# Performance work log

Hardware: AMD Instinct MI355X
Metric: run time of the kernel (lower is better)

The kernel has to match this reference:

```python
import jax, jax.numpy as jnp
import numpy as np

V = 128      # vocab size (pad=0, sos=1, eos=2)
E = 128      # embed_dim == LSTM hidden
L = 2        # rnn_layers
B = 8192     # batch (num_samples)
T = 128      # token sequence length incl. sos/eos
PAD, SOS, EOS = 0, 1, 2


def setup_inputs() -> dict:
    key = jax.random.key(0)
    ks = jax.random.split(key, 9)
    s = 1.0 / np.sqrt(E)
    state = jax.random.normal(ks[0], (B, E), dtype=jnp.float32)
    tokens = jax.random.randint(ks[1], (B, T), 3, V)
    tokens = tokens.at[:, 0].set(SOS).at[:, -1].set(EOS)
    tok_embed = jax.random.normal(ks[2], (V, E), dtype=jnp.float32)
    W_ih = jax.random.uniform(ks[3], (L, 4 * E, E), minval=-s, maxval=s, dtype=jnp.float32)
    W_hh = jax.random.uniform(ks[4], (L, 4 * E, E), minval=-s, maxval=s, dtype=jnp.float32)
    b_ih = jax.random.uniform(ks[5], (L, 4 * E), minval=-s, maxval=s, dtype=jnp.float32)
    b_hh = jax.random.uniform(ks[6], (L, 4 * E), minval=-s, maxval=s, dtype=jnp.float32)
    W_out = jax.random.uniform(ks[7], (V, E), minval=-s, maxval=s, dtype=jnp.float32)
    b_out = jax.random.uniform(ks[8], (V,), minval=-s, maxval=s, dtype=jnp.float32)
    return {"state": state, "tokens": tokens, "tok_embed": tok_embed,
            "W_ih": W_ih, "W_hh": W_hh, "b_ih": b_ih, "b_hh": b_hh,
            "W_out": W_out, "b_out": b_out}


def _lstm(x, h0, c0, W_ih, W_hh, b_ih, b_hh):
    # x: [T, B, E] time-major; h0/c0: [L, B, E]. Gate order i,f,g,o (torch).
    n_layers = W_ih.shape[0]
    hs, cs = [], []
    for l in range(n_layers):
        Wih, Whh = W_ih[l], W_hh[l]
        b = b_ih[l] + b_hh[l]
        def step(carry, xt, Wih=Wih, Whh=Whh, b=b):
            h, c = carry
            g = xt @ Wih.T + h @ Whh.T + b            # [B, 4E]
            i, f, gg, o = jnp.split(g, 4, axis=-1)
            c = jax.nn.sigmoid(f) * c + jax.nn.sigmoid(i) * jnp.tanh(gg)
            h = jax.nn.sigmoid(o) * jnp.tanh(c)
            return (h, c), h
        (h, c), x = jax.lax.scan(step, (h0[l], c0[l]), x)
        hs.append(h)
        cs.append(c)
    return x, jnp.stack(hs), jnp.stack(cs)


def reference(state, tokens, tok_embed, W_ih, W_hh, b_ih, b_hh, W_out, b_out):
    b, e = state.shape
    n_layers = W_ih.shape[0]
    zeros = jnp.zeros((n_layers, b, e), dtype=state.dtype)
    # get_init_state: one-step LSTM over state.unsqueeze(0)
    _, h0, c0 = _lstm(state[None], zeros, zeros, W_ih, W_hh, b_ih, b_hh)
    # get_likelihood (all sequences same length -> dense, no pad tokens)
    x = tok_embed[tokens.T]                               # [T, B, E]
    out, _, _ = _lstm(x, h0, c0, W_ih, W_hh, b_ih, b_hh)  # [T, B, E]
    logits = out[:-1] @ W_out.T + b_out                   # [T-1, B, V]
    targets = tokens.T[1:]                                # [T-1, B]
    lp = jax.nn.log_softmax(logits, axis=-1)
    nll = -jnp.take_along_axis(lp, targets[..., None], axis=-1)[..., 0]
    mask = (targets != PAD).astype(nll.dtype)             # ignore_index=pad
    ll = -jnp.sum(nll * mask, axis=0)[:, None]            # [B, 1]
    return ll
```

## Files before the change

### kernel.cpp

```cpp
#include <hip/hip_runtime.h>
#include <hip/hip_bf16.h>


typedef __bf16 bf16x8 __attribute__((ext_vector_type(8)));
typedef float  f32x4  __attribute__((ext_vector_type(4)));

static __device__ __bf16 g_emb1[128 * 512];

__device__ __forceinline__ float frcp(float x) {
#if __has_builtin(__builtin_amdgcn_rcpf)
  return __builtin_amdgcn_rcpf(x);
#else
  return 1.0f / x;
#endif
}
__device__ __forceinline__ float fsig(float x) { return frcp(1.0f + __expf(-x)); }
__device__ __forceinline__ float ftanh(float x) {
  float e = __expf(2.0f * x);
  return 1.0f - 2.0f * frcp(e + 1.0f);
}

__global__ void prep_emb1(const float* __restrict__ emb, const float* __restrict__ Wih,
                          const float* __restrict__ bih, const float* __restrict__ bhh) {
  __shared__ float embS[128 * 128];
  __shared__ float wS[32 * 128];
  const int tid = threadIdx.x, bc = blockIdx.x;
  for (int i = tid; i < 128 * 32; i += 512) ((f32x4*)embS)[i] = ((const f32x4*)emb)[i];
  for (int i = tid; i < 32 * 32; i += 512)
    ((f32x4*)wS)[i] = ((const f32x4*)(Wih + bc * 32 * 128))[i];
  __syncthreads();
  const int v = tid & 127, c0 = (tid >> 7) * 8;
  const int rot = v & 31;
#pragma unroll
  for (int j = 0; j < 8; ++j) {
    int c = c0 + j;
    float s = 0.f;
    for (int k = 0; k < 128; ++k) {
      int kk = (k + rot) & 127;
      s += embS[v * 128 + kk] * wS[c * 128 + kk];
    }
    int col = bc * 32 + c;
    g_emb1[v * 512 + col] = (__bf16)(s + bih[col] + bhh[col]);
  }
}

__global__ __launch_bounds__(512, 2) void lstm_ll(
    const float* __restrict__ state, const int* __restrict__ tokens,
    const float* __restrict__ W_ih, const float* __restrict__ W_hh,
    const float* __restrict__ b_ih, const float* __restrict__ b_hh,
    const float* __restrict__ W_out, const float* __restrict__ b_out,
    float* __restrict__ out) {
  __shared__ __align__(16) __bf16 wih2L[512 * 128];
  __shared__ __align__(16) __bf16 h1L[2][32 * 128];
  __shared__ __align__(16) __bf16 h2L[32 * 128];
  __shared__ unsigned char tokL[128][32];
  __shared__ float wsum[8][32];
  __shared__ float llL[32];

  const int tid  = threadIdx.x;
  const int w    = tid >> 6;
  const int lane = tid & 63;
  const int lr   = lane & 15;
  const int lh   = lane >> 4;
  const int b0   = blockIdx.x * 32;
  const int col  = w * 16 + lr;

  for (int i = tid; i < 512 * 16; i += 512) {
    int row = i >> 4, e = (i & 15) * 8;
    const float* p = W_ih + 512 * 128 + row * 128 + e;
    f32x4 x0 = *(const f32x4*)p, x1 = *(const f32x4*)(p + 4);
    bf16x8 v;
#pragma unroll
    for (int j = 0; j < 4; ++j) { v[j] = (__bf16)x0[j]; v[4 + j] = (__bf16)x1[j]; }
    *(bf16x8*)(wih2L + row * 128 + (e ^ ((row & 7) << 3))) = v;
  }
  for (int i = tid; i < 32 * 128; i += 512) {
    int r = i & 31, t = i >> 5;
    tokL[t][r] = (unsigned char)tokens[(b0 + r) * 128 + t];
    h2L[i] = (__bf16)0.0f;
  }
  if (tid < 32) llL[tid] = 0.0f;

  auto ldw8 = [&](const float* p) -> bf16x8 {
    f32x4 x0 = *(const f32x4*)p, x1 = *(const f32x4*)(p + 4);
    bf16x8 v;
#pragma unroll
    for (int j = 0; j < 4; ++j) { v[j] = (__bf16)x0[j]; v[4 + j] = (__bf16)x1[j]; }
    return v;
  };
  bf16x8 whh1[4][4], whh2[4][4], woutF[4];
#pragma unroll
  for (int kc = 0; kc < 4; ++kc) {
#pragma unroll
    for (int gg = 0; gg < 4; ++gg) {
      whh1[kc][gg] = ldw8(W_hh + (gg * 128 + col) * 128 + kc * 32 + lh * 8);
      whh2[kc][gg] = ldw8(W_hh + 512 * 128 + (gg * 128 + col) * 128 + kc * 32 + lh * 8);
    }
    woutF[kc] = ldw8(W_out + col * 128 + kc * 32 + lh * 8);
  }
  float bias1v[4], bias2v[4];
#pragma unroll
  for (int gg = 0; gg < 4; ++gg) {
    bias1v[gg] = b_ih[gg * 128 + col] + b_hh[gg * 128 + col];
    bias2v[gg] = b_ih[512 + gg * 128 + col] + b_hh[512 + gg * 128 + col];
  }
  const float bo = b_out[col];
  float c1[2][4] = {}, c2[2][4] = {};
  const float z4[4] = {0.f, 0.f, 0.f, 0.f};

  f32x4 acc[2][4];
  auto zacc = [&]() {
#pragma unroll
    for (int mf = 0; mf < 2; ++mf)
#pragma unroll
      for (int gg = 0; gg < 4; ++gg) acc[mf][gg] = f32x4{0.f, 0.f, 0.f, 0.f};
  };
  auto ldsA = [&](const __bf16* buf, int row, int kc) -> bf16x8 {
    return *(const bf16x8*)(buf + row * 128 + ((kc * 32 + lh * 8) ^ ((row & 7) << 3)));
  };

  auto g2phase = [&](const __bf16* h1cur) {
    zacc();
#pragma unroll
    for (int kc = 0; kc < 4; ++kc) {
      bf16x8 a0 = ldsA(h1cur, lr, kc), a1 = ldsA(h1cur, 16 + lr, kc);
      bf16x8 d0 = ldsA(h2L, lr, kc), d1 = ldsA(h2L, 16 + lr, kc);
#pragma unroll
      for (int gg = 0; gg < 4; ++gg) {
        bf16x8 bi = *(const bf16x8*)(wih2L + (gg * 128 + col) * 128 +
                                     ((kc * 32 + lh * 8) ^ ((col & 7) << 3)));
        acc[0][gg] = __builtin_amdgcn_mfma_f32_16x16x32_bf16(a0, bi, acc[0][gg], 0, 0, 0);
        acc[1][gg] = __builtin_amdgcn_mfma_f32_16x16x32_bf16(a1, bi, acc[1][gg], 0, 0, 0);
        acc[0][gg] = __builtin_amdgcn_mfma_f32_16x16x32_bf16(d0, whh2[kc][gg], acc[0][gg], 0, 0, 0);
        acc[1][gg] = __builtin_amdgcn_mfma_f32_16x16x32_bf16(d1, whh2[kc][gg], acc[1][gg], 0, 0, 0);
      }
    }
  };

  auto elem = [&](const float* b4, float (&c)[2][4], __bf16* hout) {
#pragma unroll
    for (int mf = 0; mf < 2; ++mf)
#pragma unroll
      for (int j = 0; j < 4; ++j) {
        float gi = acc[mf][0][j] + b4[0];
        float gf = acc[mf][1][j] + b4[1];
        float gc = acc[mf][2][j] + b4[2];
        float go = acc[mf][3][j] + b4[3];
        float cc = fsig(gf) * c[mf][j] + fsig(gi) * ftanh(gc);
        c[mf][j] = cc;
        float h = fsig(go) * ftanh(cc);
        int r = mf * 16 + lh * 4 + j;
        hout[r * 128 + (col ^ ((r & 7) << 3))] = (__bf16)h;
      }
  };

  auto logits = [&](int t) {
    f32x4 la[2];
    la[0] = f32x4{0.f, 0.f, 0.f, 0.f};
    la[1] = f32x4{0.f, 0.f, 0.f, 0.f};
#pragma unroll
    for (int kc = 0; kc < 4; ++kc) {
      bf16x8 a0 = ldsA(h2L, lr, kc), a1 = ldsA(h2L, 16 + lr, kc);
      la[0] = __builtin_amdgcn_mfma_f32_16x16x32_bf16(a0, woutF[kc], la[0], 0, 0, 0);
      la[1] = __builtin_amdgcn_mfma_f32_16x16x32_bf16(a1, woutF[kc], la[1], 0, 0, 0);
    }
    float lv[2][4];
#pragma unroll
    for (int mf = 0; mf < 2; ++mf)
#pragma unroll
      for (int j = 0; j < 4; ++j) {
        float v = la[mf][j] + bo;
        lv[mf][j] = v;
        float s = __expf(v);
        s += __shfl_xor(s, 1);
        s += __shfl_xor(s, 2);
        s += __shfl_xor(s, 4);
        s += __shfl_xor(s, 8);
        if (lr == 0) wsum[w][mf * 16 + lh * 4 + j] = s;
      }
    __syncthreads();
#pragma unroll
    for (int mf = 0; mf < 2; ++mf)
#pragma unroll
      for (int j = 0; j < 4; ++j) {
        int r = mf * 16 + lh * 4 + j;
        int tgt = (int)tokL[t + 1][r];
        if ((tgt >> 4) == w && (tgt & 15) == lr) {
          float S = 0.f;
#pragma unroll
          for (int ww = 0; ww < 8; ++ww) S += wsum[ww][r];
          llL[r] += lv[mf][j] - __logf(S);
        }
      }
  };

  __syncthreads();

  {
    zacc();
#pragma unroll
    for (int kc = 0; kc < 4; ++kc) {
      const float* p0 = state + (size_t)(b0 + lr) * 128 + kc * 32 + lh * 8;
      const float* p1 = state + (size_t)(b0 + 16 + lr) * 128 + kc * 32 + lh * 8;
      bf16x8 a0 = ldw8(p0), a1 = ldw8(p1);
#pragma unroll
      for (int gg = 0; gg < 4; ++gg) {
        bf16x8 bw = ldw8(W_ih + (gg * 128 + col) * 128 + kc * 32 + lh * 8);
        acc[0][gg] = __builtin_amdgcn_mfma_f32_16x16x32_bf16(a0, bw, acc[0][gg], 0, 0, 0);
        acc[1][gg] = __builtin_amdgcn_mfma_f32_16x16x32_bf16(a1, bw, acc[1][gg], 0, 0, 0);
      }
    }
    elem(bias1v, c1, h1L[0]);
    __syncthreads();
    g2phase(h1L[0]);
    __syncthreads();
    elem(bias2v, c2, h2L);
    __syncthreads();
  }

#pragma unroll 1
  for (int t = 0; t < 127; ++t) {
    const __bf16* h1p = h1L[t & 1];
    __bf16* h1c = h1L[(t & 1) ^ 1];

    __bf16 gv[2][4][4];
#pragma unroll
    for (int mf = 0; mf < 2; ++mf)
#pragma unroll
      for (int j = 0; j < 4; ++j) {
        int tk = (int)tokL[t][mf * 16 + lh * 4 + j];
#pragma unroll
        for (int gg = 0; gg < 4; ++gg) gv[mf][gg][j] = g_emb1[tk * 512 + gg * 128 + col];
      }
    zacc();
#pragma unroll
    for (int kc = 0; kc < 4; ++kc) {
      bf16x8 a0 = ldsA(h1p, lr, kc), a1 = ldsA(h1p, 16 + lr, kc);
#pragma unroll
      for (int gg = 0; gg < 4; ++gg) {
        acc[0][gg] = __builtin_amdgcn_mfma_f32_16x16x32_bf16(a0, whh1[kc][gg], acc[0][gg], 0, 0, 0);
        acc[1][gg] = __builtin_amdgcn_mfma_f32_16x16x32_bf16(a1, whh1[kc][gg], acc[1][gg], 0, 0, 0);
      }
    }
#pragma unroll
    for (int mf = 0; mf < 2; ++mf)
#pragma unroll
      for (int gg = 0; gg < 4; ++gg)
#pragma unroll
        for (int j = 0; j < 4; ++j) acc[mf][gg][j] += (float)gv[mf][gg][j];
    elem(z4, c1, h1c);
    __syncthreads();

    g2phase(h1c);
    __syncthreads();
    elem(bias2v, c2, h2L);
    __syncthreads();

    logits(t);
  }

  __syncthreads();
  if (tid < 32) out[b0 + tid] = llL[tid];
}

extern "C" void kernel_launch(void* const* d_in, const int* in_sizes, int n_in,
                              void* d_out, int out_size, void* d_ws, size_t ws_size,
                              hipStream_t stream) {
  const float* state  = (const float*)d_in[0];
  const int*   tokens = (const int*)d_in[1];
  const float* emb    = (const float*)d_in[2];
  const float* Wih    = (const float*)d_in[3];
  const float* Whh    = (const float*)d_in[4];
  const float* bih    = (const float*)d_in[5];
  const float* bhh    = (const float*)d_in[6];
  const float* Wout   = (const float*)d_in[7];
  const float* bout   = (const float*)d_in[8];
  float* out = (float*)d_out;

  prep_emb1<<<16, 512, 0, stream>>>(emb, Wih, bih, bhh);
  lstm_ll<<<256, 512, 0, stream>>>(state, tokens, Wih, Whh, bih, bhh, Wout, bout, out);
}
```

Before: 1.224 ms.

## Pipeline logits with LSTM steps, fold exp2 scaling into weights, transpose MFMA

```diff
diff --git a/kernel.cpp b/kernel.cpp
--- a/kernel.cpp
+++ b/kernel.cpp
@@ -3,7 +3,11 @@
 
 
 typedef __bf16 bf16x8 __attribute__((ext_vector_type(8)));
+typedef __bf16 bf16x4 __attribute__((ext_vector_type(4)));
 typedef float  f32x4  __attribute__((ext_vector_type(4)));
+
+#define LOG2E 1.4426950408889634f
+#define LN2   0.6931471805599453f
 
 static __device__ __bf16 g_emb1[128 * 512];
 
@@ -14,10 +18,19 @@
   return 1.0f / x;
 #endif
 }
-__device__ __forceinline__ float fsig(float x) { return frcp(1.0f + __expf(-x)); }
-__device__ __forceinline__ float ftanh(float x) {
-  float e = __expf(2.0f * x);
-  return 1.0f - 2.0f * frcp(e + 1.0f);
+__device__ __forceinline__ float fexp2(float x) {
+#if __has_builtin(__builtin_amdgcn_exp2f)
+  return __builtin_amdgcn_exp2f(x);
+#else
+  return exp2f(x);
+#endif
+}
+__device__ __forceinline__ float flog2(float x) {
+#if __has_builtin(__builtin_amdgcn_logf)
+  return __builtin_amdgcn_logf(x);
+#else
+  return log2f(x);
+#endif
 }
 
 __global__ void prep_emb1(const float* __restrict__ emb, const float* __restrict__ Wih,
@@ -40,7 +53,8 @@
       s += embS[v * 128 + kk] * wS[c * 128 + kk];
     }
     int col = bc * 32 + c;
-    g_emb1[v * 512 + col] = (__bf16)(s + bih[col] + bhh[col]);
+    float sc = ((col >> 7) == 2) ? 2.0f * LOG2E : LOG2E;
+    g_emb1[v * 512 + col] = (__bf16)((s + bih[col] + bhh[col]) * sc);
   }
 }
 
@@ -64,203 +78,231 @@
   const int lh   = lane >> 4;
   const int b0   = blockIdx.x * 32;
   const int col  = w * 16 + lr;
+  const int koff = lh * 8;
+  const int e0   = w * 16 + lh * 4;
+  const float gscA[4] = {LOG2E, LOG2E, 2.0f * LOG2E, LOG2E};
+  const int sw = (lr & 7) << 3;
 
   for (int i = tid; i < 512 * 16; i += 512) {
     int row = i >> 4, e = (i & 15) * 8;
     const float* p = W_ih + 512 * 128 + row * 128 + e;
+    float sc = gscA[row >> 7];
     f32x4 x0 = *(const f32x4*)p, x1 = *(const f32x4*)(p + 4);
     bf16x8 v;
 #pragma unroll
-    for (int j = 0; j < 4; ++j) { v[j] = (__bf16)x0[j]; v[4 + j] = (__bf16)x1[j]; }
+    for (int j = 0; j < 4; ++j) { v[j] = (__bf16)(x0[j] * sc); v[4 + j] = (__bf16)(x1[j] * sc); }
     *(bf16x8*)(wih2L + row * 128 + (e ^ ((row & 7) << 3))) = v;
   }
   for (int i = tid; i < 32 * 128; i += 512) {
     int r = i & 31, t = i >> 5;
     tokL[t][r] = (unsigned char)tokens[(b0 + r) * 128 + t];
-    h2L[i] = (__bf16)0.0f;
   }
   if (tid < 32) llL[tid] = 0.0f;
 
-  auto ldw8 = [&](const float* p) -> bf16x8 {
+  auto ldw8s = [&](const float* p, float sc) -> bf16x8 {
     f32x4 x0 = *(const f32x4*)p, x1 = *(const f32x4*)(p + 4);
     bf16x8 v;
 #pragma unroll
-    for (int j = 0; j < 4; ++j) { v[j] = (__bf16)x0[j]; v[4 + j] = (__bf16)x1[j]; }
+    for (int j = 0; j < 4; ++j) { v[j] = (__bf16)(x0[j] * sc); v[4 + j] = (__bf16)(x1[j] * sc); }
     return v;
   };
+
   bf16x8 whh1[4][4], whh2[4][4], woutF[4];
 #pragma unroll
   for (int kc = 0; kc < 4; ++kc) {
 #pragma unroll
     for (int gg = 0; gg < 4; ++gg) {
-      whh1[kc][gg] = ldw8(W_hh + (gg * 128 + col) * 128 + kc * 32 + lh * 8);
-      whh2[kc][gg] = ldw8(W_hh + 512 * 128 + (gg * 128 + col) * 128 + kc * 32 + lh * 8);
-    }
-    woutF[kc] = ldw8(W_out + col * 128 + kc * 32 + lh * 8);
-  }
-  float bias1v[4], bias2v[4];
-#pragma unroll
-  for (int gg = 0; gg < 4; ++gg) {
-    bias1v[gg] = b_ih[gg * 128 + col] + b_hh[gg * 128 + col];
-    bias2v[gg] = b_ih[512 + gg * 128 + col] + b_hh[512 + gg * 128 + col];
-  }
-  const float bo = b_out[col];
+      whh1[kc][gg] = ldw8s(W_hh + (gg * 128 + col) * 128 + kc * 32 + koff, gscA[gg]);
+      whh2[kc][gg] = ldw8s(W_hh + 512 * 128 + (gg * 128 + col) * 128 + kc * 32 + koff, gscA[gg]);
+    }
+    woutF[kc] = ldw8s(W_out + col * 128 + kc * 32 + koff, LOG2E);
+  }
+  f32x4 bias2v4[4], bo4;
+#pragma unroll
+  for (int gg = 0; gg < 4; ++gg)
+#pragma unroll
+    for (int j = 0; j < 4; ++j)
+      bias2v4[gg][j] = (b_ih[512 + gg * 128 + e0 + j] + b_hh[512 + gg * 128 + e0 + j]) * gscA[gg];
+#pragma unroll
+  for (int j = 0; j < 4; ++j) bo4[j] = b_out[e0 + j] * LOG2E;
+
   float c1[2][4] = {}, c2[2][4] = {};
-  const float z4[4] = {0.f, 0.f, 0.f, 0.f};
-
-  f32x4 acc[2][4];
+
+  auto ldB = [&](const __bf16* buf, int nf, int kc) -> bf16x8 {
+    return *(const bf16x8*)(buf + (nf * 16 + lr) * 128 + ((kc * 32 + koff) ^ sw));
+  };
+
+  f32x4 acc[4][2];
   auto zacc = [&]() {
 #pragma unroll
-    for (int mf = 0; mf < 2; ++mf)
-#pragma unroll
-      for (int gg = 0; gg < 4; ++gg) acc[mf][gg] = f32x4{0.f, 0.f, 0.f, 0.f};
-  };
-  auto ldsA = [&](const __bf16* buf, int row, int kc) -> bf16x8 {
-    return *(const bf16x8*)(buf + row * 128 + ((kc * 32 + lh * 8) ^ ((row & 7) << 3)));
-  };
-
-  auto g2phase = [&](const __bf16* h1cur) {
-    zacc();
-#pragma unroll
-    for (int kc = 0; kc < 4; ++kc) {
-      bf16x8 a0 = ldsA(h1cur, lr, kc), a1 = ldsA(h1cur, 16 + lr, kc);
-      bf16x8 d0 = ldsA(h2L, lr, kc), d1 = ldsA(h2L, 16 + lr, kc);
-#pragma unroll
-      for (int gg = 0; gg < 4; ++gg) {
-        bf16x8 bi = *(const bf16x8*)(wih2L + (gg * 128 + col) * 128 +
-                                     ((kc * 32 + lh * 8) ^ ((col & 7) << 3)));
-        acc[0][gg] = __builtin_amdgcn_mfma_f32_16x16x32_bf16(a0, bi, acc[0][gg], 0, 0, 0);
-        acc[1][gg] = __builtin_amdgcn_mfma_f32_16x16x32_bf16(a1, bi, acc[1][gg], 0, 0, 0);
-        acc[0][gg] = __builtin_amdgcn_mfma_f32_16x16x32_bf16(d0, whh2[kc][gg], acc[0][gg], 0, 0, 0);
-        acc[1][gg] = __builtin_amdgcn_mfma_f32_16x16x32_bf16(d1, whh2[kc][gg], acc[1][gg], 0, 0, 0);
-      }
-    }
-  };
-
-  auto elem = [&](const float* b4, float (&c)[2][4], __bf16* hout) {
-#pragma unroll
-    for (int mf = 0; mf < 2; ++mf)
+    for (int gg = 0; gg < 4; ++gg)
+#pragma unroll
+      for (int nf = 0; nf < 2; ++nf) acc[gg][nf] = f32x4{0.f, 0.f, 0.f, 0.f};
+  };
+
+  auto elem = [&](const f32x4* b4, float (&c)[2][4], __bf16* hout) {
+#pragma unroll
+    for (int nf = 0; nf < 2; ++nf) {
+      bf16x4 hp;
 #pragma unroll
       for (int j = 0; j < 4; ++j) {
-        float gi = acc[mf][0][j] + b4[0];
-        float gf = acc[mf][1][j] + b4[1];
-        float gc = acc[mf][2][j] + b4[2];
-        float go = acc[mf][3][j] + b4[3];
-        float cc = fsig(gf) * c[mf][j] + fsig(gi) * ftanh(gc);
-        c[mf][j] = cc;
-        float h = fsig(go) * ftanh(cc);
-        int r = mf * 16 + lh * 4 + j;
-        hout[r * 128 + (col ^ ((r & 7) << 3))] = (__bf16)h;
-      }
-  };
-
-  auto logits = [&](int t) {
-    f32x4 la[2];
-    la[0] = f32x4{0.f, 0.f, 0.f, 0.f};
-    la[1] = f32x4{0.f, 0.f, 0.f, 0.f};
-#pragma unroll
-    for (int kc = 0; kc < 4; ++kc) {
-      bf16x8 a0 = ldsA(h2L, lr, kc), a1 = ldsA(h2L, 16 + lr, kc);
-      la[0] = __builtin_amdgcn_mfma_f32_16x16x32_bf16(a0, woutF[kc], la[0], 0, 0, 0);
-      la[1] = __builtin_amdgcn_mfma_f32_16x16x32_bf16(a1, woutF[kc], la[1], 0, 0, 0);
-    }
-    float lv[2][4];
-#pragma unroll
-    for (int mf = 0; mf < 2; ++mf)
-#pragma unroll
-      for (int j = 0; j < 4; ++j) {
-        float v = la[mf][j] + bo;
-        lv[mf][j] = v;
-        float s = __expf(v);
-        s += __shfl_xor(s, 1);
-        s += __shfl_xor(s, 2);
-        s += __shfl_xor(s, 4);
-        s += __shfl_xor(s, 8);
-        if (lr == 0) wsum[w][mf * 16 + lh * 4 + j] = s;
-      }
-    __syncthreads();
-#pragma unroll
-    for (int mf = 0; mf < 2; ++mf)
-#pragma unroll
-      for (int j = 0; j < 4; ++j) {
-        int r = mf * 16 + lh * 4 + j;
-        int tgt = (int)tokL[t + 1][r];
-        if ((tgt >> 4) == w && (tgt & 15) == lr) {
-          float S = 0.f;
-#pragma unroll
-          for (int ww = 0; ww < 8; ++ww) S += wsum[ww][r];
-          llL[r] += lv[mf][j] - __logf(S);
-        }
-      }
-  };
+        float gi = acc[0][nf][j] + b4[0][j];
+        float gf = acc[1][nf][j] + b4[1][j];
+        float gc = acc[2][nf][j] + b4[2][j];
+        float go = acc[3][nf][j] + b4[3][j];
+        float sf = frcp(1.f + fexp2(-gf));
+        float si = frcp(1.f + fexp2(-gi));
+        float tg = 1.f - 2.f * frcp(fexp2(gc) + 1.f);
+        float cc = sf * c[nf][j] + si * tg;
+        c[nf][j] = cc;
+        float so = frcp(1.f + fexp2(-go));
+        float tc = 1.f - 2.f * frcp(fexp2(2.f * LOG2E * cc) + 1.f);
+        hp[j] = (__bf16)(so * tc);
+      }
+      int b = nf * 16 + lr;
+      *(bf16x4*)(hout + b * 128 + (e0 ^ ((b & 7) << 3))) = hp;
+    }
+  };
+  const f32x4 zf4 = {0.f, 0.f, 0.f, 0.f};
+  const f32x4 zb4[4] = {zf4, zf4, zf4, zf4};
 
   __syncthreads();
+
+  bf16x4 gv[2][4];
+  auto gather = [&](int t) {
+#pragma unroll
+    for (int nf = 0; nf < 2; ++nf) {
+      int tk = (int)tokL[t][nf * 16 + lr];
+      const __bf16* pp = g_emb1 + tk * 512 + e0;
+#pragma unroll
+      for (int gg = 0; gg < 4; ++gg) gv[nf][gg] = *(const bf16x4*)(pp + gg * 128);
+    }
+  };
+  gather(0);
 
   {
     zacc();
 #pragma unroll
     for (int kc = 0; kc < 4; ++kc) {
-      const float* p0 = state + (size_t)(b0 + lr) * 128 + kc * 32 + lh * 8;
-      const float* p1 = state + (size_t)(b0 + 16 + lr) * 128 + kc * 32 + lh * 8;
-      bf16x8 a0 = ldw8(p0), a1 = ldw8(p1);
+      bf16x8 s0 = ldw8s(state + (size_t)(b0 + lr) * 128 + kc * 32 + koff, 1.0f);
+      bf16x8 s1 = ldw8s(state + (size_t)(b0 + 16 + lr) * 128 + kc * 32 + koff, 1.0f);
 #pragma unroll
       for (int gg = 0; gg < 4; ++gg) {
-        bf16x8 bw = ldw8(W_ih + (gg * 128 + col) * 128 + kc * 32 + lh * 8);
-        acc[0][gg] = __builtin_amdgcn_mfma_f32_16x16x32_bf16(a0, bw, acc[0][gg], 0, 0, 0);
-        acc[1][gg] = __builtin_amdgcn_mfma_f32_16x16x32_bf16(a1, bw, acc[1][gg], 0, 0, 0);
-      }
-    }
-    elem(bias1v, c1, h1L[0]);
-    __syncthreads();
-    g2phase(h1L[0]);
-    __syncthreads();
-    elem(bias2v, c2, h2L);
-    __syncthreads();
-  }
+        bf16x8 a = ldw8s(W_ih + (gg * 128 + col) * 128 + kc * 32 + koff, gscA[gg]);
+        acc[gg][0] = __builtin_amdgcn_mfma_f32_16x16x32_bf16(a, s0, acc[gg][0], 0, 0, 0);
+        acc[gg][1] = __builtin_amdgcn_mfma_f32_16x16x32_bf16(a, s1, acc[gg][1], 0, 0, 0);
+      }
+    }
+    f32x4 bias1v4[4];
+#pragma unroll
+    for (int gg = 0; gg < 4; ++gg)
+#pragma unroll
+      for (int j = 0; j < 4; ++j)
+        bias1v4[gg][j] = (b_ih[gg * 128 + e0 + j] + b_hh[gg * 128 + e0 + j]) * gscA[gg];
+    elem(bias1v4, c1, h1L[0]);
+    __syncthreads();
+    zacc();
+#pragma unroll
+    for (int kc = 0; kc < 4; ++kc) {
+      bf16x8 x0 = ldB(h1L[0], 0, kc), x1 = ldB(h1L[0], 1, kc);
+#pragma unroll
+      for (int gg = 0; gg < 4; ++gg) {
+        bf16x8 a = *(const bf16x8*)(wih2L + (gg * 128 + col) * 128 + ((kc * 32 + koff) ^ sw));
+        acc[gg][0] = __builtin_amdgcn_mfma_f32_16x16x32_bf16(a, x0, acc[gg][0], 0, 0, 0);
+        acc[gg][1] = __builtin_amdgcn_mfma_f32_16x16x32_bf16(a, x1, acc[gg][1], 0, 0, 0);
+      }
+    }
+    elem(bias2v4, c2, h2L);
+    __syncthreads();
+  }
+
+  f32x4 lvA, lvB;
 
 #pragma unroll 1
-  for (int t = 0; t < 127; ++t) {
+  for (int t = 0; t <= 127; ++t) {
+    const bool act = (t < 127), pend = (t > 0);
     const __bf16* h1p = h1L[t & 1];
     __bf16* h1c = h1L[(t & 1) ^ 1];
 
-    __bf16 gv[2][4][4];
-#pragma unroll
-    for (int mf = 0; mf < 2; ++mf)
-#pragma unroll
-      for (int j = 0; j < 4; ++j) {
-        int tk = (int)tokL[t][mf * 16 + lh * 4 + j];
-#pragma unroll
-        for (int gg = 0; gg < 4; ++gg) gv[mf][gg][j] = g_emb1[tk * 512 + gg * 128 + col];
-      }
-    zacc();
-#pragma unroll
-    for (int kc = 0; kc < 4; ++kc) {
-      bf16x8 a0 = ldsA(h1p, lr, kc), a1 = ldsA(h1p, 16 + lr, kc);
-#pragma unroll
-      for (int gg = 0; gg < 4; ++gg) {
-        acc[0][gg] = __builtin_amdgcn_mfma_f32_16x16x32_bf16(a0, whh1[kc][gg], acc[0][gg], 0, 0, 0);
-        acc[1][gg] = __builtin_amdgcn_mfma_f32_16x16x32_bf16(a1, whh1[kc][gg], acc[1][gg], 0, 0, 0);
-      }
-    }
-#pragma unroll
-    for (int mf = 0; mf < 2; ++mf)
-#pragma unroll
-      for (int gg = 0; gg < 4; ++gg)
-#pragma unroll
-        for (int j = 0; j < 4; ++j) acc[mf][gg][j] += (float)gv[mf][gg][j];
-    elem(z4, c1, h1c);
-    __syncthreads();
-
-    g2phase(h1c);
-    __syncthreads();
-    elem(bias2v, c2, h2L);
-    __syncthreads();
-
-    logits(t);
-  }
-
-  __syncthreads();
-  if (tid < 32) out[b0 + tid] = llL[tid];
+    if (pend) {
+      f32x4 la0 = zf4, la1 = zf4;
+#pragma unroll
+      for (int kc = 0; kc < 4; ++kc) {
+        bf16x8 y0 = ldB(h2L, 0, kc), y1 = ldB(h2L, 1, kc);
+        la0 = __builtin_amdgcn_mfma_f32_16x16x32_bf16(woutF[kc], y0, la0, 0, 0, 0);
+        la1 = __builtin_amdgcn_mfma_f32_16x16x32_bf16(woutF[kc], y1, la1, 0, 0, 0);
+      }
+      lvA = la0 + bo4;
+      lvB = la1 + bo4;
+    }
+    if (act) {
+      zacc();
+#pragma unroll
+      for (int kc = 0; kc < 4; ++kc) {
+        bf16x8 p0 = ldB(h1p, 0, kc), p1 = ldB(h1p, 1, kc);
+#pragma unroll
+        for (int gg = 0; gg < 4; ++gg) {
+          acc[gg][0] = __builtin_amdgcn_mfma_f32_16x16x32_bf16(whh1[kc][gg], p0, acc[gg][0], 0, 0, 0);
+          acc[gg][1] = __builtin_amdgcn_mfma_f32_16x16x32_bf16(whh1[kc][gg], p1, acc[gg][1], 0, 0, 0);
+        }
+      }
+#pragma unroll
+      for (int nf = 0; nf < 2; ++nf)
+#pragma unroll
+        for (int gg = 0; gg < 4; ++gg)
+#pragma unroll
+          for (int j = 0; j < 4; ++j) acc[gg][nf][j] += (float)gv[nf][gg][j];
+    }
+    if (pend) {
+      float s0 = fexp2(lvA[0]) + fexp2(lvA[1]) + fexp2(lvA[2]) + fexp2(lvA[3]);
+      float s1 = fexp2(lvB[0]) + fexp2(lvB[1]) + fexp2(lvB[2]) + fexp2(lvB[3]);
+      s0 += __shfl_xor(s0, 16); s0 += __shfl_xor(s0, 32);
+      s1 += __shfl_xor(s1, 16); s1 += __shfl_xor(s1, 32);
+      if (lh == 0) { wsum[w][lr] = s0; wsum[w][16 + lr] = s1; }
+    }
+    if (act) elem(zb4, c1, h1c);
+    __syncthreads();
+
+    if (act) {
+      if (t + 1 < 127) gather(t + 1);
+      zacc();
+#pragma unroll
+      for (int kc = 0; kc < 4; ++kc) {
+        bf16x8 x0 = ldB(h1c, 0, kc), x1 = ldB(h1c, 1, kc);
+        bf16x8 y0 = ldB(h2L, 0, kc), y1 = ldB(h2L, 1, kc);
+#pragma unroll
+        for (int gg = 0; gg < 4; ++gg) {
+          bf16x8 a = *(const bf16x8*)(wih2L + (gg * 128 + col) * 128 + ((kc * 32 + koff) ^ sw));
+          acc[gg][0] = __builtin_amdgcn_mfma_f32_16x16x32_bf16(a, x0, acc[gg][0], 0, 0, 0);
+          acc[gg][1] = __builtin_amdgcn_mfma_f32_16x16x32_bf16(a, x1, acc[gg][1], 0, 0, 0);
+          acc[gg][0] = __builtin_amdgcn_mfma_f32_16x16x32_bf16(whh2[kc][gg], y0, acc[gg][0], 0, 0, 0);
+          acc[gg][1] = __builtin_amdgcn_mfma_f32_16x16x32_bf16(whh2[kc][gg], y1, acc[gg][1], 0, 0, 0);
+        }
+      }
+    }
+    if (pend) {
+#pragma unroll
+      for (int nf = 0; nf < 2; ++nf) {
+        int r = nf * 16 + lr;
+        int tgt = (int)tokL[t][r];
+        if ((tgt >> 4) == w && ((tgt >> 2) & 3) == lh) {
+          int j = tgt & 3;
+          const f32x4& lv = nf ? lvB : lvA;
+          float lvs = (j & 2) ? ((j & 1) ? lv[3] : lv[2]) : ((j & 1) ? lv[1] : lv[0]);
+          float S = 0.f;
+#pragma unroll
+          for (int ww = 0; ww < 8; ++ww) S += wsum[ww][r];
+          llL[r] += lvs - flog2(S);
+        }
+      }
+    }
+    __syncthreads();
+
+    if (act) elem(bias2v4, c2, h2L);
+    __syncthreads();
+  }
+
+  if (tid < 32) out[b0 + tid] = llL[tid] * LN2;
 }
 
 extern "C" void kernel_launch(void* const* d_in, const int* in_sizes, int n_in,
```

Measured after the change: 1.128 ms. -7.9%, faster.
